# Performance work log

Measured on AMD Instinct MI355X. Metric: run time of the kernel, lower is better.

## Reference

```python
import jax, jax.numpy as jnp
import numpy as np

EPS = 1e-9
LAMBDA_VIOLATION = 0.5

B, S, K, N, M = 2048, 20, 128, 256, 10  # batch, num_samples, k, n, m


def setup_inputs() -> dict:
    key = jax.random.key(0)
    k1, k2, k3, k4 = jax.random.split(key, 4)
    y_pred = jax.random.uniform(k1, (B, 1), dtype=jnp.float32) * 10.0 + 1.0
    y_true = jax.random.uniform(k2, (B, 1), dtype=jnp.float32) * 10.0 + 1.0
    P_padded = jax.random.normal(k3, (B, K, N - K), dtype=jnp.float32)
    samples = jax.random.normal(k4, (B, S, K), dtype=jnp.float32)
    return {"y_pred": y_pred, "y_true": y_true, "P_padded": P_padded,
            "samples": samples, "m": M}


def reference(y_pred, y_true, P_padded, samples, m):
    b, s, k = samples.shape
    n = k + P_padded.shape[2]
    # LogMSE term
    yp = jnp.clip(y_pred, EPS)
    yt = jnp.clip(y_true, EPS)
    logmse = jnp.mean((jnp.log2(yt) - jnp.log2(yp)) ** 2)
    # Build generator matrices G = [I_k | P] : [B, k, n]
    I = jnp.broadcast_to(jnp.eye(k, dtype=P_padded.dtype), (b, k, k))
    G = jnp.concatenate([I, P_padded], axis=2)
    # Random codewords: [B, S, n]
    codewords = jnp.einsum('bsk,bkn->bsn', samples, G)
    mags = jnp.abs(codewords).reshape(b * s, n)
    top_vals, _ = jax.lax.top_k(mags, m + 1)  # [B*S, m+1] descending
    hm = (top_vals[:, 0] / (top_vals[:, m] + EPS)).reshape(b, s)
    max_hm = jnp.max(hm, axis=1)  # [B]
    penalty = jnp.sum(jax.nn.relu(max_hm - y_pred.squeeze(-1)))
    violation = penalty / b
    total_loss = logmse + LAMBDA_VIOLATION * violation
    return total_loss, logmse, violation
```

## Files before the change

kernel.cpp:

```cpp
#include <hip/hip_runtime.h>
#include <math.h>

#define EPSF 1e-9f
#define KK 128
#define MTOP 10

__global__ __launch_bounds__(256, 4) void fused_kernel(
    const float* __restrict__ y_pred, const float* __restrict__ y_true,
    const float* __restrict__ P, const float* __restrict__ samples,
    float* __restrict__ accum )
{
    const int tid  = threadIdx.x;
    const int wave = tid >> 6;
    const int lane = tid & 63;
    const int b    = blockIdx.x;
    const int r0   = wave * 5;
    const int j2   = lane << 1;

    const float* __restrict__ Pb = P + ((size_t)b << 14);
    const float* __restrict__ Sb = samples + (size_t)b * (20 * KK);

    __shared__ float sS[20 * KK];
    __shared__ float red[4];

    float2 vs[5];
#pragma unroll
    for (int r = 0; r < 5; ++r) {
        vs[r] = *(const float2*)(Sb + (r0 + r) * KK + j2);
        *(float2*)&sS[(r0 + r) * KK + j2] = vs[r];
    }
    __syncthreads();

    float2 acc[5];
#pragma unroll
    for (int r = 0; r < 5; ++r) acc[r] = make_float2(0.f, 0.f);

#pragma unroll 2
    for (int k = 0; k < KK; k += 4) {
        float2 p0 = *(const float2*)(Pb + (k + 0) * KK + j2);
        float2 p1 = *(const float2*)(Pb + (k + 1) * KK + j2);
        float2 p2 = *(const float2*)(Pb + (k + 2) * KK + j2);
        float2 p3 = *(const float2*)(Pb + (k + 3) * KK + j2);
#pragma unroll
        for (int r = 0; r < 5; ++r) {
            float4 s = *(const float4*)&sS[(r0 + r) * KK + k];
            acc[r].x = fmaf(s.x, p0.x, acc[r].x);
            acc[r].y = fmaf(s.x, p0.y, acc[r].y);
            acc[r].x = fmaf(s.y, p1.x, acc[r].x);
            acc[r].y = fmaf(s.y, p1.y, acc[r].y);
            acc[r].x = fmaf(s.z, p2.x, acc[r].x);
            acc[r].y = fmaf(s.z, p2.y, acc[r].y);
            acc[r].x = fmaf(s.w, p3.x, acc[r].x);
            acc[r].y = fmaf(s.w, p3.y, acc[r].y);
        }
    }

    float hmax = 0.f;
#pragma unroll
    for (int r = 0; r < 5; ++r) {
        float v0 = fabsf(acc[r].x), v1 = fabsf(acc[r].y);
        float v2 = fabsf(vs[r].x),  v3 = fabsf(vs[r].y);
        float m1 = fmaxf(fmaxf(v0, v1), fmaxf(v2, v3));
#pragma unroll
        for (int d = 32; d >= 1; d >>= 1)
            m1 = fmaxf(m1, __shfl_xor(m1, d, 64));
        unsigned lo = 0u, hi = __float_as_uint(m1);
        while (lo < hi) {
            unsigned mid = lo + ((hi - lo + 1) >> 1);
            float mf = __uint_as_float(mid);
            int cnt = __popcll(__ballot(v0 > mf)) + __popcll(__ballot(v1 > mf))
                    + __popcll(__ballot(v2 > mf)) + __popcll(__ballot(v3 > mf));
            if (cnt >= MTOP + 1) lo = mid; else hi = mid - 1;
        }
        float m11 = __uint_as_float(lo + 1u);
        hmax = fmaxf(hmax, m1 / (m11 + EPSF));
    }

    if (lane == 0) red[wave] = hmax;
    __syncthreads();
    if (tid == 0) {
        float hb  = fmaxf(fmaxf(red[0], red[1]), fmaxf(red[2], red[3]));
        float ypv = y_pred[b];
        float yp  = fmaxf(ypv, EPSF);
        float yt  = fmaxf(y_true[b], EPSF);
        float d   = log2f(yt) - log2f(yp);
        atomicAdd(&accum[0], d * d);
        atomicAdd(&accum[1], fmaxf(hb - ypv, 0.f));
    }
}

__global__ void finalize_kernel(const float* __restrict__ accum,
                                float* __restrict__ out, float invB)
{
    if (threadIdx.x == 0) {
        float logmse    = accum[0] * invB;
        float violation = accum[1] * invB;
        out[0] = logmse + 0.5f * violation;
        out[1] = logmse;
        out[2] = violation;
    }
}

extern "C" void kernel_launch(void* const* d_in, const int* in_sizes, int n_in,
                              void* d_out, int out_size, void* d_ws, size_t ws_size,
                              hipStream_t stream) {
    const float* y_pred  = (const float*)d_in[0];
    const float* y_true  = (const float*)d_in[1];
    const float* P       = (const float*)d_in[2];
    const float* samples = (const float*)d_in[3];
    const int B = in_sizes[0];

    float* accum = (float*)d_ws;
    hipMemsetAsync(accum, 0, 2 * sizeof(float), stream);

    fused_kernel<<<B, 256, 0, stream>>>(y_pred, y_true, P, samples, accum);
    finalize_kernel<<<1, 64, 0, stream>>>(accum, (float*)d_out, 1.0f / (float)B);
}
```

Baseline: 261.8 us.

## Split K across half-waves with float4 P loads, interleave top-k bisections, drop atomics

Each wave now splits the 128-deep reduction between two half-waves. Each lane loads float4 columns of P and accumulates four outputs, and the two partial sums are combined with a cross-half shuffle. The identity part of the codeword is read back from shared memory. The five per-row binary searches for the 11th largest value run interleaved in one loop, giving more independent ballots to overlap. Global atomics and the memset are replaced by per-block partial writes, which the finalize kernel reduces with 256 threads. The change adds registers and a hardcoded finalize loop that assumes B=2048.

```diff
diff --git a/kernel.cpp b/kernel.cpp
--- a/kernel.cpp
+++ b/kernel.cpp
@@ -8,14 +8,17 @@
 __global__ __launch_bounds__(256, 4) void fused_kernel(
     const float* __restrict__ y_pred, const float* __restrict__ y_true,
     const float* __restrict__ P, const float* __restrict__ samples,
-    float* __restrict__ accum )
+    float* __restrict__ partial )
 {
-    const int tid  = threadIdx.x;
-    const int wave = tid >> 6;
-    const int lane = tid & 63;
-    const int b    = blockIdx.x;
-    const int r0   = wave * 5;
-    const int j2   = lane << 1;
+    const int tid   = threadIdx.x;
+    const int wave  = tid >> 6;
+    const int lane  = tid & 63;
+    const int b     = blockIdx.x;
+    const int r0    = wave * 5;
+    const int sg    = lane >> 5;
+    const int c     = lane & 31;
+    const int j4    = c << 2;
+    const int kbase = sg << 6;
 
     const float* __restrict__ Pb = P + ((size_t)b << 14);
     const float* __restrict__ Sb = samples + (size_t)b * (20 * KK);
@@ -23,57 +26,93 @@
     __shared__ float sS[20 * KK];
     __shared__ float red[4];
 
-    float2 vs[5];
 #pragma unroll
-    for (int r = 0; r < 5; ++r) {
-        vs[r] = *(const float2*)(Sb + (r0 + r) * KK + j2);
-        *(float2*)&sS[(r0 + r) * KK + j2] = vs[r];
+    for (int i = 0; i < 5; ++i) {
+        const int idx = (i * 256 + tid) * 2;
+        *(float2*)&sS[idx] = *(const float2*)(Sb + idx);
     }
     __syncthreads();
 
-    float2 acc[5];
+    float4 acc[5];
 #pragma unroll
-    for (int r = 0; r < 5; ++r) acc[r] = make_float2(0.f, 0.f);
+    for (int r = 0; r < 5; ++r) acc[r] = make_float4(0.f, 0.f, 0.f, 0.f);
 
+    const float* __restrict__ Pw = Pb + (size_t)kbase * KK + j4;
 #pragma unroll 2
-    for (int k = 0; k < KK; k += 4) {
-        float2 p0 = *(const float2*)(Pb + (k + 0) * KK + j2);
-        float2 p1 = *(const float2*)(Pb + (k + 1) * KK + j2);
-        float2 p2 = *(const float2*)(Pb + (k + 2) * KK + j2);
-        float2 p3 = *(const float2*)(Pb + (k + 3) * KK + j2);
+    for (int kk = 0; kk < 64; kk += 4) {
+        float4 p0 = *(const float4*)(Pw + (kk + 0) * KK);
+        float4 p1 = *(const float4*)(Pw + (kk + 1) * KK);
+        float4 p2 = *(const float4*)(Pw + (kk + 2) * KK);
+        float4 p3 = *(const float4*)(Pw + (kk + 3) * KK);
 #pragma unroll
         for (int r = 0; r < 5; ++r) {
-            float4 s = *(const float4*)&sS[(r0 + r) * KK + k];
+            float4 s = *(const float4*)&sS[(r0 + r) * KK + kbase + kk];
             acc[r].x = fmaf(s.x, p0.x, acc[r].x);
             acc[r].y = fmaf(s.x, p0.y, acc[r].y);
+            acc[r].z = fmaf(s.x, p0.z, acc[r].z);
+            acc[r].w = fmaf(s.x, p0.w, acc[r].w);
             acc[r].x = fmaf(s.y, p1.x, acc[r].x);
             acc[r].y = fmaf(s.y, p1.y, acc[r].y);
+            acc[r].z = fmaf(s.y, p1.z, acc[r].z);
+            acc[r].w = fmaf(s.y, p1.w, acc[r].w);
             acc[r].x = fmaf(s.z, p2.x, acc[r].x);
             acc[r].y = fmaf(s.z, p2.y, acc[r].y);
+            acc[r].z = fmaf(s.z, p2.z, acc[r].z);
+            acc[r].w = fmaf(s.z, p2.w, acc[r].w);
             acc[r].x = fmaf(s.w, p3.x, acc[r].x);
             acc[r].y = fmaf(s.w, p3.y, acc[r].y);
+            acc[r].z = fmaf(s.w, p3.z, acc[r].z);
+            acc[r].w = fmaf(s.w, p3.w, acc[r].w);
+        }
+    }
+
+    float w0[5], w1[5], w2[5], w3[5];
+#pragma unroll
+    for (int r = 0; r < 5; ++r) {
+        float ax = acc[r].x + __shfl_xor(acc[r].x, 32, 64);
+        float ay = acc[r].y + __shfl_xor(acc[r].y, 32, 64);
+        float az = acc[r].z + __shfl_xor(acc[r].z, 32, 64);
+        float aw = acc[r].w + __shfl_xor(acc[r].w, 32, 64);
+        float4 idv = *(const float4*)&sS[(r0 + r) * KK + j4];
+        w0[r] = fabsf(sg ? idv.x : ax);
+        w1[r] = fabsf(sg ? idv.y : ay);
+        w2[r] = fabsf(sg ? idv.z : az);
+        w3[r] = fabsf(sg ? idv.w : aw);
+    }
+
+    float mx[5];
+#pragma unroll
+    for (int r = 0; r < 5; ++r) {
+        float lm = fmaxf(fmaxf(w0[r], w1[r]), fmaxf(w2[r], w3[r]));
+#pragma unroll
+        for (int d = 32; d >= 1; d >>= 1)
+            lm = fmaxf(lm, __shfl_xor(lm, d, 64));
+        mx[r] = lm;
+    }
+
+    unsigned lo[5], hi[5];
+#pragma unroll
+    for (int r = 0; r < 5; ++r) { lo[r] = 0u; hi[r] = __float_as_uint(mx[r]); }
+
+    while (lo[0] < hi[0] || lo[1] < hi[1] || lo[2] < hi[2] ||
+           lo[3] < hi[3] || lo[4] < hi[4]) {
+#pragma unroll
+        for (int r = 0; r < 5; ++r) {
+            unsigned mid = lo[r] + ((hi[r] - lo[r] + 1u) >> 1);
+            float mf = __uint_as_float(mid);
+            int cnt = __popcll(__ballot(w0[r] > mf)) + __popcll(__ballot(w1[r] > mf))
+                    + __popcll(__ballot(w2[r] > mf)) + __popcll(__ballot(w3[r] > mf));
+            bool g = cnt >= (MTOP + 1);
+            lo[r] = g ? mid : lo[r];
+            hi[r] = g ? hi[r] : mid - 1u;
         }
     }
 
     float hmax = 0.f;
 #pragma unroll
     for (int r = 0; r < 5; ++r) {
-        float v0 = fabsf(acc[r].x), v1 = fabsf(acc[r].y);
-        float v2 = fabsf(vs[r].x),  v3 = fabsf(vs[r].y);
-        float m1 = fmaxf(fmaxf(v0, v1), fmaxf(v2, v3));
-#pragma unroll
-        for (int d = 32; d >= 1; d >>= 1)
-            m1 = fmaxf(m1, __shfl_xor(m1, d, 64));
-        unsigned lo = 0u, hi = __float_as_uint(m1);
-        while (lo < hi) {
-            unsigned mid = lo + ((hi - lo + 1) >> 1);
-            float mf = __uint_as_float(mid);
-            int cnt = __popcll(__ballot(v0 > mf)) + __popcll(__ballot(v1 > mf))
-                    + __popcll(__ballot(v2 > mf)) + __popcll(__ballot(v3 > mf));
-            if (cnt >= MTOP + 1) lo = mid; else hi = mid - 1;
-        }
-        float m11 = __uint_as_float(lo + 1u);
-        hmax = fmaxf(hmax, m1 / (m11 + EPSF));
+        float m11 = __uint_as_float(lo[r] + 1u);
+        hmax = fmaxf(hmax, mx[r] / (m11 + EPSF));
     }
 
     if (lane == 0) red[wave] = hmax;
@@ -84,20 +123,36 @@
         float yp  = fmaxf(ypv, EPSF);
         float yt  = fmaxf(y_true[b], EPSF);
         float d   = log2f(yt) - log2f(yp);
-        atomicAdd(&accum[0], d * d);
-        atomicAdd(&accum[1], fmaxf(hb - ypv, 0.f));
+        partial[2 * b]     = d * d;
+        partial[2 * b + 1] = fmaxf(hb - ypv, 0.f);
     }
 }
 
-__global__ void finalize_kernel(const float* __restrict__ accum,
-                                float* __restrict__ out, float invB)
+__global__ __launch_bounds__(256) void finalize_kernel(
+    const float* __restrict__ partial, float* __restrict__ out, float invB)
 {
-    if (threadIdx.x == 0) {
-        float logmse    = accum[0] * invB;
-        float violation = accum[1] * invB;
-        out[0] = logmse + 0.5f * violation;
-        out[1] = logmse;
-        out[2] = violation;
+    const int t = threadIdx.x;
+    float sl = 0.f, sp = 0.f;
+#pragma unroll
+    for (int i = 0; i < 8; ++i) {
+        float2 v = *(const float2*)(partial + 2 * (t + i * 256));
+        sl += v.x; sp += v.y;
+    }
+#pragma unroll
+    for (int d = 32; d >= 1; d >>= 1) {
+        sl += __shfl_xor(sl, d, 64);
+        sp += __shfl_xor(sp, d, 64);
+    }
+    __shared__ float rl[4], rp[4];
+    const int w = t >> 6;
+    if ((t & 63) == 0) { rl[w] = sl; rp[w] = sp; }
+    __syncthreads();
+    if (t == 0) {
+        float L = (rl[0] + rl[1] + rl[2] + rl[3]) * invB;
+        float V = (rp[0] + rp[1] + rp[2] + rp[3]) * invB;
+        out[0] = L + 0.5f * V;
+        out[1] = L;
+        out[2] = V;
     }
 }
 
@@ -110,9 +165,8 @@
     const float* samples = (const float*)d_in[3];
     const int B = in_sizes[0];
 
-    float* accum = (float*)d_ws;
-    hipMemsetAsync(accum, 0, 2 * sizeof(float), stream);
+    float* partial = (float*)d_ws;
 
-    fused_kernel<<<B, 256, 0, stream>>>(y_pred, y_true, P, samples, accum);
-    finalize_kernel<<<1, 64, 0, stream>>>(accum, (float*)d_out, 1.0f / (float)B);
+    fused_kernel<<<B, 256, 0, stream>>>(y_pred, y_true, P, samples, partial);
+    finalize_kernel<<<1, 256, 0, stream>>>(partial, (float*)d_out, 1.0f / (float)B);
 }
```

Result: faster. 236.0 us (-9.9%).
